# Performance work log

Hardware: AMD Instinct MI355X
Metric: run time of the kernel (lower is better)

## Reference

```python
import jax, jax.numpy as jnp
import numpy as np

B, S, I, F = 2048, 512, 256, 256  # batch, seq_length, input_size, filter_num


def setup_inputs() -> dict:
    key = jax.random.key(0)
    ks = jax.random.split(key, 9)
    sc = 0.05
    return {
        "hidden": jax.random.normal(ks[0], (B, I), jnp.float32),
        "inp": jax.random.normal(ks[1], (B, S, I), jnp.float32),
        "W1": jax.random.normal(ks[2], (F, I), jnp.float32) * sc,   # linear1 weight (no bias)
        "Wc": jax.random.normal(ks[3], (F, S), jnp.float32) * sc,   # conv kernel [F,1,S,1] squeezed
        "bc": jax.random.normal(ks[4], (F,), jnp.float32) * sc,     # conv bias
        "W2": jax.random.normal(ks[5], (I, I + F), jnp.float32) * sc,
        "b2": jax.random.normal(ks[6], (I,), jnp.float32) * sc,
        "Wfc": jax.random.normal(ks[7], (1, I), jnp.float32) * sc,
        "bfc": jax.random.normal(ks[8], (1,), jnp.float32) * sc,
    }


def reference(hidden, inp, W1, Wc, bc, W2, b2, Wfc, bfc):
    # w = linear1(hidden).unsqueeze(1): [B,1,F]
    w = hidden @ W1.T  # [B,F]
    # Conv2d(1,F,kernel=(S,1)) over input [B,1,S,I] -> [B,F,1,I]; kernel spans full
    # time axis with width 1, so it's a contraction over t per input channel i.
    Hc_raw = jnp.einsum('bti,ft->bfi', inp, Wc) + bc[None, :, None]  # [B,F,I]
    # faithful to torch: .squeeze().reshape([-1, input_size, filter_num])
    H_c = Hc_raw.reshape(-1, I, F)  # [B,I,F]
    s = jnp.sum(H_c * w[:, None, :], axis=2)          # [B,I]
    a = jax.nn.sigmoid(s)
    v = jnp.sum(a[:, :, None] * H_c, axis=1)          # [B,F]
    concat = jnp.concatenate([hidden, v], axis=1)     # [B,I+F]
    h_prime = concat @ W2.T + b2                      # [B,I]
    out = h_prime @ Wfc.T + bfc                       # [B,1]
    return out
```

## Files before the change

kernel.cpp:

```cpp
#include <hip/hip_runtime.h>

#define B_ 2048
#define S_ 512
#define I_ 256
#define F_ 256

#define OFF_R    0
#define OFF_C0   512
#define OFF_RS   513
#define OFF_W    1024
#define OFF_SW   (OFF_W + B_*F_)
#define OFF_U    (OFF_SW + B_)
#define OFF_P    (OFF_U + B_*S_)

__global__ __launch_bounds__(512) void k0_fold(
    const float* __restrict__ W2, const float* __restrict__ b2,
    const float* __restrict__ Wfc, const float* __restrict__ bfc,
    float* __restrict__ ws) {
  const int j = threadIdx.x;
  float acc = 0.f;
#pragma unroll 8
  for (int i = 0; i < I_; ++i) acc += Wfc[i] * W2[i * (I_ + F_) + j];
  ws[OFF_R + j] = acc;

  __shared__ float red[512];
  red[j] = (j < I_) ? Wfc[j] * b2[j] : 0.f;
  __syncthreads();
  for (int s = 256; s > 0; s >>= 1) { if (j < s) red[j] += red[j + s]; __syncthreads(); }
  if (j == 0) ws[OFF_C0] = red[0] + bfc[0];
  __syncthreads();
  red[j] = (j >= I_) ? acc : 0.f;
  __syncthreads();
  for (int s = 256; s > 0; s >>= 1) { if (j < s) red[j] += red[j + s]; __syncthreads(); }
  if (j == 0) ws[OFF_RS] = red[0];
}

__global__ __launch_bounds__(256) void kw_lin1(
    const float* __restrict__ hidden, const float* __restrict__ W1,
    float* __restrict__ ws) {
  const int b0 = blockIdx.x * 4;
  const int tid = threadIdx.x;
  __shared__ float h[4][I_];
#pragma unroll
  for (int k = 0; k < 4; ++k) h[k][tid] = hidden[(size_t)(b0 + k) * I_ + tid];
  __syncthreads();

  const int f = tid;
  const float4* wrow = (const float4*)(W1 + (size_t)f * I_);
  float acc[4] = {0.f, 0.f, 0.f, 0.f};
#pragma unroll 4
  for (int iq = 0; iq < I_ / 4; ++iq) {
    const float4 v = wrow[iq];
    const int i = 4 * iq;
#pragma unroll
    for (int k = 0; k < 4; ++k)
      acc[k] += v.x * h[k][i] + v.y * h[k][i + 1] + v.z * h[k][i + 2] + v.w * h[k][i + 3];
  }
#pragma unroll
  for (int k = 0; k < 4; ++k) ws[OFF_W + (size_t)(b0 + k) * F_ + f] = acc[k];

  __shared__ float red[256];
#pragma unroll
  for (int k = 0; k < 4; ++k) {
    red[tid] = acc[k];
    __syncthreads();
    for (int s = 128; s > 0; s >>= 1) { if (tid < s) red[tid] += red[tid + s]; __syncthreads(); }
    if (tid == 0) ws[OFF_SW + b0 + k] = red[0];
    __syncthreads();
  }
}

__global__ __launch_bounds__(256) void k1_scan(
    const float* __restrict__ inp, float* __restrict__ ws) {
  const int ROWS = 32;
  const int b = blockIdx.y;
  const int t0 = blockIdx.x * ROWS;
  const int lane = threadIdx.x & 63;
  const int wid = threadIdx.x >> 6;

  const float4 w4  = ((const float4*)(ws + OFF_W + (size_t)b * F_))[lane];
  const float4 rv4 = ((const float4*)(ws + OFF_R + 256))[lane];
  const float* base = inp + ((size_t)b * S_ + t0) * I_;
  float* uo = ws + OFF_U + (size_t)b * S_ + t0;
  float* po = ws + OFF_P + (size_t)b * S_ + t0;

#pragma unroll
  for (int rr = 0; rr < ROWS / 4; ++rr) {
    const int row = wid + 4 * rr;
    const float4 in4 = ((const float4*)(base + (size_t)row * I_))[lane];
    float du = in4.x * w4.x + in4.y * w4.y + in4.z * w4.z + in4.w * w4.w;
    float dp = in4.x * rv4.x + in4.y * rv4.y + in4.z * rv4.z + in4.w * rv4.w;
#pragma unroll
    for (int m = 32; m >= 1; m >>= 1) {
      du += __shfl_xor(du, m, 64);
      dp += __shfl_xor(dp, m, 64);
    }
    if (lane == 0) { uo[row] = du; po[row] = dp; }
  }
}

__global__ __launch_bounds__(256) void k2_epilogue(
    const float* __restrict__ Wc, const float* __restrict__ bc,
    const float* __restrict__ hidden, const float* __restrict__ ws,
    float* __restrict__ out) {
  const int b0 = blockIdx.x * 4;
  const int tid = threadIdx.x;
  __shared__ float u[4][S_];
  __shared__ float p[4][S_];
  const float* wsu = ws + OFF_U;
  const float* wsp = ws + OFF_P;
#pragma unroll
  for (int k = 0; k < 4; ++k) {
    u[k][tid]       = wsu[(size_t)(b0 + k) * S_ + tid];
    u[k][tid + 256] = wsu[(size_t)(b0 + k) * S_ + tid + 256];
    p[k][tid]       = wsp[(size_t)(b0 + k) * S_ + tid];
    p[k][tid + 256] = wsp[(size_t)(b0 + k) * S_ + tid + 256];
  }
  __syncthreads();

  const int x = tid;
  const float4* wrow = (const float4*)(Wc + (size_t)x * S_);
  float ss[4] = {0.f, 0.f, 0.f, 0.f};
  float qs[4] = {0.f, 0.f, 0.f, 0.f};
#pragma unroll 4
  for (int tq = 0; tq < S_ / 4; ++tq) {
    const float4 v = wrow[tq];
    const int t = 4 * tq;
#pragma unroll
    for (int k = 0; k < 4; ++k) {
      ss[k] += v.x * u[k][t] + v.y * u[k][t + 1] + v.z * u[k][t + 2] + v.w * u[k][t + 3];
      qs[k] += v.x * p[k][t] + v.y * p[k][t + 1] + v.z * p[k][t + 2] + v.w * p[k][t + 3];
    }
  }

  const float bcx = bc[x];
  const float R   = ws[OFF_RS];
  const float rh  = ws[OFF_R + x];
  const float c0  = ws[OFF_C0];

  __shared__ float red[256];
#pragma unroll
  for (int k = 0; k < 4; ++k) {
    const float Sw = ws[OFF_SW + b0 + k];
    const float s  = ss[k] + bcx * Sw;
    const float a  = 1.f / (1.f + expf(-s));
    float partial  = a * (qs[k] + bcx * R) + rh * hidden[(size_t)(b0 + k) * I_ + x];
    red[tid] = partial;
    __syncthreads();
    for (int st = 128; st > 0; st >>= 1) { if (tid < st) red[tid] += red[tid + st]; __syncthreads(); }
    if (tid == 0) out[b0 + k] = red[0] + c0;
    __syncthreads();
  }
}

extern "C" void kernel_launch(void* const* d_in, const int* in_sizes, int n_in,
                              void* d_out, int out_size, void* d_ws, size_t ws_size,
                              hipStream_t stream) {
  (void)in_sizes; (void)n_in; (void)out_size; (void)ws_size;
  const float* hidden = (const float*)d_in[0];
  const float* inp    = (const float*)d_in[1];
  const float* W1     = (const float*)d_in[2];
  const float* Wc     = (const float*)d_in[3];
  const float* bc     = (const float*)d_in[4];
  const float* W2     = (const float*)d_in[5];
  const float* b2     = (const float*)d_in[6];
  const float* Wfc    = (const float*)d_in[7];
  const float* bfc    = (const float*)d_in[8];
  float* out = (float*)d_out;
  float* ws  = (float*)d_ws;

  hipLaunchKernelGGL(k0_fold, dim3(1), dim3(512), 0, stream, W2, b2, Wfc, bfc, ws);
  hipLaunchKernelGGL(kw_lin1, dim3(B_ / 4), dim3(256), 0, stream, hidden, W1, ws);
  hipLaunchKernelGGL(k1_scan, dim3(S_ / 32, B_), dim3(256), 0, stream, inp, ws);
  hipLaunchKernelGGL(k2_epilogue, dim3(B_ / 4), dim3(256), 0, stream, Wc, bc, hidden, ws, out);
}
```

Measured before the change: 279.9 us.

## Merge fold and linear1 kernels, widen scan rows, use wave-shuffle epilogue reduction

```diff
diff --git a/kernel.cpp b/kernel.cpp
--- a/kernel.cpp
+++ b/kernel.cpp
@@ -13,34 +13,40 @@
 #define OFF_U    (OFF_SW + B_)
 #define OFF_P    (OFF_U + B_*S_)
 
-__global__ __launch_bounds__(512) void k0_fold(
+__global__ __launch_bounds__(256) void k_pre(
+    const float* __restrict__ hidden, const float* __restrict__ W1,
     const float* __restrict__ W2, const float* __restrict__ b2,
     const float* __restrict__ Wfc, const float* __restrict__ bfc,
     float* __restrict__ ws) {
-  const int j = threadIdx.x;
-  float acc = 0.f;
+  __shared__ float h[4][I_];
+  __shared__ float red[256];
+  const int tid = threadIdx.x;
+
+  if (blockIdx.x == B_ / 4) {
+    const int j = tid;
+    float acc0 = 0.f, acc1 = 0.f;
 #pragma unroll 8
-  for (int i = 0; i < I_; ++i) acc += Wfc[i] * W2[i * (I_ + F_) + j];
-  ws[OFF_R + j] = acc;
+    for (int i = 0; i < I_; ++i) {
+      const float f = Wfc[i];
+      acc0 += f * W2[(size_t)i * (I_ + F_) + j];
+      acc1 += f * W2[(size_t)i * (I_ + F_) + j + 256];
+    }
+    ws[OFF_R + j] = acc0;
+    ws[OFF_R + 256 + j] = acc1;
 
-  __shared__ float red[512];
-  red[j] = (j < I_) ? Wfc[j] * b2[j] : 0.f;
-  __syncthreads();
-  for (int s = 256; s > 0; s >>= 1) { if (j < s) red[j] += red[j + s]; __syncthreads(); }
-  if (j == 0) ws[OFF_C0] = red[0] + bfc[0];
-  __syncthreads();
-  red[j] = (j >= I_) ? acc : 0.f;
-  __syncthreads();
-  for (int s = 256; s > 0; s >>= 1) { if (j < s) red[j] += red[j + s]; __syncthreads(); }
-  if (j == 0) ws[OFF_RS] = red[0];
-}
+    red[j] = Wfc[j] * b2[j];
+    __syncthreads();
+    for (int s = 128; s > 0; s >>= 1) { if (j < s) red[j] += red[j + s]; __syncthreads(); }
+    if (j == 0) ws[OFF_C0] = red[0] + bfc[0];
+    __syncthreads();
+    red[j] = acc1;
+    __syncthreads();
+    for (int s = 128; s > 0; s >>= 1) { if (j < s) red[j] += red[j + s]; __syncthreads(); }
+    if (j == 0) ws[OFF_RS] = red[0];
+    return;
+  }
 
-__global__ __launch_bounds__(256) void kw_lin1(
-    const float* __restrict__ hidden, const float* __restrict__ W1,
-    float* __restrict__ ws) {
   const int b0 = blockIdx.x * 4;
-  const int tid = threadIdx.x;
-  __shared__ float h[4][I_];
 #pragma unroll
   for (int k = 0; k < 4; ++k) h[k][tid] = hidden[(size_t)(b0 + k) * I_ + tid];
   __syncthreads();
@@ -59,7 +65,6 @@
 #pragma unroll
   for (int k = 0; k < 4; ++k) ws[OFF_W + (size_t)(b0 + k) * F_ + f] = acc[k];
 
-  __shared__ float red[256];
 #pragma unroll
   for (int k = 0; k < 4; ++k) {
     red[tid] = acc[k];
@@ -72,30 +77,40 @@
 
 __global__ __launch_bounds__(256) void k1_scan(
     const float* __restrict__ inp, float* __restrict__ ws) {
-  const int ROWS = 32;
   const int b = blockIdx.y;
-  const int t0 = blockIdx.x * ROWS;
+  const int t0 = blockIdx.x * 64;
   const int lane = threadIdx.x & 63;
   const int wid = threadIdx.x >> 6;
+  const int c = lane & 15;
+  const int rg = lane >> 4;
 
-  const float4 w4  = ((const float4*)(ws + OFF_W + (size_t)b * F_))[lane];
-  const float4 rv4 = ((const float4*)(ws + OFF_R + 256))[lane];
+  float4 w4[4], rv4[4];
+  const float4* wptr = (const float4*)(ws + OFF_W + (size_t)b * F_);
+  const float4* rvptr = (const float4*)(ws + OFF_R + 256);
+#pragma unroll
+  for (int j = 0; j < 4; ++j) { w4[j] = wptr[c * 4 + j]; rv4[j] = rvptr[c * 4 + j]; }
+
   const float* base = inp + ((size_t)b * S_ + t0) * I_;
   float* uo = ws + OFF_U + (size_t)b * S_ + t0;
   float* po = ws + OFF_P + (size_t)b * S_ + t0;
 
 #pragma unroll
-  for (int rr = 0; rr < ROWS / 4; ++rr) {
-    const int row = wid + 4 * rr;
-    const float4 in4 = ((const float4*)(base + (size_t)row * I_))[lane];
-    float du = in4.x * w4.x + in4.y * w4.y + in4.z * w4.z + in4.w * w4.w;
-    float dp = in4.x * rv4.x + in4.y * rv4.y + in4.z * rv4.z + in4.w * rv4.w;
+  for (int g = 0; g < 4; ++g) {
+    const int row = wid * 16 + g * 4 + rg;
+    const float4* rbase = (const float4*)(base + (size_t)row * I_ + c * 16);
+    float du = 0.f, dp = 0.f;
 #pragma unroll
-    for (int m = 32; m >= 1; m >>= 1) {
+    for (int j = 0; j < 4; ++j) {
+      const float4 v = rbase[j];
+      du += v.x * w4[j].x + v.y * w4[j].y + v.z * w4[j].z + v.w * w4[j].w;
+      dp += v.x * rv4[j].x + v.y * rv4[j].y + v.z * rv4[j].z + v.w * rv4[j].w;
+    }
+#pragma unroll
+    for (int m = 8; m >= 1; m >>= 1) {
       du += __shfl_xor(du, m, 64);
       dp += __shfl_xor(dp, m, 64);
     }
-    if (lane == 0) { uo[row] = du; po[row] = dp; }
+    if (c == 0) { uo[row] = du; po[row] = dp; }
   }
 }
 
@@ -105,8 +120,11 @@
     float* __restrict__ out) {
   const int b0 = blockIdx.x * 4;
   const int tid = threadIdx.x;
+  const int lane = tid & 63;
+  const int wid = tid >> 6;
   __shared__ float u[4][S_];
   __shared__ float p[4][S_];
+  __shared__ float wred[4][4];
   const float* wsu = ws + OFF_U;
   const float* wsp = ws + OFF_P;
 #pragma unroll
@@ -134,23 +152,23 @@
   }
 
   const float bcx = bc[x];
-  const float R   = ws[OFF_RS];
-  const float rh  = ws[OFF_R + x];
-  const float c0  = ws[OFF_C0];
+  const float R = ws[OFF_RS];
+  const float rh = ws[OFF_R + x];
+  const float c0 = ws[OFF_C0];
 
-  __shared__ float red[256];
 #pragma unroll
   for (int k = 0; k < 4; ++k) {
     const float Sw = ws[OFF_SW + b0 + k];
-    const float s  = ss[k] + bcx * Sw;
-    const float a  = 1.f / (1.f + expf(-s));
-    float partial  = a * (qs[k] + bcx * R) + rh * hidden[(size_t)(b0 + k) * I_ + x];
-    red[tid] = partial;
-    __syncthreads();
-    for (int st = 128; st > 0; st >>= 1) { if (tid < st) red[tid] += red[tid + st]; __syncthreads(); }
-    if (tid == 0) out[b0 + k] = red[0] + c0;
-    __syncthreads();
+    const float s = ss[k] + bcx * Sw;
+    const float a = 1.f / (1.f + expf(-s));
+    float partial = a * (qs[k] + bcx * R) + rh * hidden[(size_t)(b0 + k) * I_ + x];
+#pragma unroll
+    for (int m = 32; m >= 1; m >>= 1) partial += __shfl_xor(partial, m, 64);
+    if (lane == 0) wred[k][wid] = partial;
   }
+  __syncthreads();
+  if (tid < 4)
+    out[b0 + tid] = wred[tid][0] + wred[tid][1] + wred[tid][2] + wred[tid][3] + c0;
 }
 
 extern "C" void kernel_launch(void* const* d_in, const int* in_sizes, int n_in,
@@ -169,8 +187,8 @@
   float* out = (float*)d_out;
   float* ws  = (float*)d_ws;
 
-  hipLaunchKernelGGL(k0_fold, dim3(1), dim3(512), 0, stream, W2, b2, Wfc, bfc, ws);
-  hipLaunchKernelGGL(kw_lin1, dim3(B_ / 4), dim3(256), 0, stream, hidden, W1, ws);
-  hipLaunchKernelGGL(k1_scan, dim3(S_ / 32, B_), dim3(256), 0, stream, inp, ws);
+  hipLaunchKernelGGL(k_pre, dim3(B_ / 4 + 1), dim3(256), 0, stream,
+                     hidden, W1, W2, b2, Wfc, bfc, ws);
+  hipLaunchKernelGGL(k1_scan, dim3(S_ / 64, B_), dim3(256), 0, stream, inp, ws);
   hipLaunchKernelGGL(k2_epilogue, dim3(B_ / 4), dim3(256), 0, stream, Wc, bc, hidden, ws, out);
 }
```

Result: slower. 287.7 us (+2.8%).
